# Kernel tuning notes

Measured on AMD Instinct MI355X. Metric: run time of the kernel, lower is better.

Reference implementation:

```python
import jax, jax.numpy as jnp
import numpy as np

T, C, H, W = 16, 3, 512, 512
PS, PT = 7, 1
NQ = 262144


def setup_inputs() -> dict:
    key = jax.random.key(0)
    k1, k2, k3, k4 = jax.random.split(key, 4)
    vid2fill = jnp.zeros((T, C, H, W), jnp.float32)
    patches = jax.random.normal(k1, (NQ, PT, C, PS, PS), jnp.float32)
    # queryInds columns: (t, h, w) top-left corners, each kept in-bounds
    qt = jax.random.randint(k2, (NQ, 1), 0, T - PT + 1)
    qh = jax.random.randint(k3, (NQ, 1), 0, H - PS + 1)
    qw = jax.random.randint(k4, (NQ, 1), 0, W - PS + 1)
    queryInds = jnp.concatenate([qt, qh, qw], axis=1).astype(jnp.int32)
    return {"vid2fill": vid2fill, "patches": patches, "queryInds": queryInds}


def reference(vid2fill, patches, queryInds):
    # vid2fill: [T,C,H,W]; patches: [N,pt,C,ps,ps]; queryInds: [N,3] = (t,h,w)
    T_, C_, H_, W_ = vid2fill.shape
    N, pt, _, ps, _ = patches.shape
    ti = queryInds[:, 0, None] + jnp.arange(pt)  # [N,pt]
    hi = queryInds[:, 1, None] + jnp.arange(ps)  # [N,ps]
    wi = queryInds[:, 2, None] + jnp.arange(ps)  # [N,ps]
    # flat spatial-temporal index over (t,h,w): [N,pt,ps,ps]
    flat = (ti[:, :, None, None] * H_ + hi[:, None, :, None]) * W_ + wi[:, None, None, :]
    # channels-last flat video [T*H*W, C] for a single vectorized scatter-add
    vid_flat = vid2fill.transpose(0, 2, 3, 1).reshape(-1, C_)
    p = patches.transpose(0, 1, 3, 4, 2).reshape(-1, C_)  # [N*pt*ps*ps, C]
    out = vid_flat.at[flat.reshape(-1)].add(p)
    return out.reshape(T_, H_, W_, C_).transpose(0, 3, 1, 2)
```

## Files before the change

### kernel.cpp

```cpp
#include <hip/hip_runtime.h>

constexpr int T_ = 16, C_ = 3, H_ = 512, W_ = 512, PS_ = 7;
constexpr int PATCH_ELEMS = C_ * PS_ * PS_;
constexpr int TILE  = 32;
constexpr int HALO  = PS_ - 1;
constexpr int LTILE = TILE + HALO;
constexpr int LSTRIDE = 40;
constexpr int NTH = H_ / TILE, NTW = W_ / TILE;
constexpr int NBINS = T_ * NTH * NTW;
constexpr int LDS_PER_C  = LTILE * LSTRIDE;
constexpr int ACC_FLOATS = C_ * LDS_PER_C;
constexpr int CAP = 160;
constexpr int BTHR = 192;
constexpr int CSTR = 16;
constexpr int NEX = 26 * 26;
constexpr int NSH = 192 + 156 + 420;

constexpr size_t OFF_COUNTS = 0;
constexpr size_t OFF_LIST   = (size_t)NBINS * CSTR * 4;
constexpr size_t WS_NEEDED  = OFF_LIST + (size_t)NBINS * CAP * 4;

__global__ void zero_counts_kernel(int* counts) {
    counts[blockIdx.x * 1024 + threadIdx.x] = 0;
}

__global__ void scatter_kernel(const int* __restrict__ q, int* __restrict__ counts,
                               int* __restrict__ list, int nq) {
    int n = blockIdx.x * 256 + threadIdx.x;
    if (n >= nq) return;
    int t = q[3 * n], h = q[3 * n + 1], w = q[3 * n + 2];
    int bin = (t * NTH + (h >> 5)) * NTW + (w >> 5);
    int pos = atomicAdd(counts + bin * CSTR, 1);
    if (pos < CAP) list[bin * CAP + pos] = (n << 10) | ((h & 31) << 5) | (w & 31);
}

__global__ __launch_bounds__(BTHR, 6) void accum_kernel(
    const float* __restrict__ patches, const int* __restrict__ counts,
    const int* __restrict__ list, float* __restrict__ out) {
    __shared__ float acc[ACC_FLOATS];
    __shared__ int recs[CAP];
    const int bin = blockIdx.x;
    const int t = bin >> 8;
    const int h0 = ((bin >> 4) & 15) * TILE, w0 = (bin & 15) * TILE;
    const int tid = threadIdx.x;
    const int lane = tid & 63, wid = tid >> 6;

    for (int i = tid; i < ACC_FLOATS; i += BTHR) acc[i] = 0.f;
    int cnt = counts[bin * CSTR];
    if (cnt > CAP) cnt = CAP;
    if (tid < cnt) recs[tid] = list[bin * CAP + tid];
    __syncthreads();

    {
        const int c = wid;
        const bool act = lane < PS_ * PS_;
        const int loff = act ? (lane / PS_) * LSTRIDE + (lane % PS_) : 0;
        float* __restrict__ ac = acc + c * LDS_PER_C;
        const float* __restrict__ pc = patches + c * (PS_ * PS_);

        float v0=0,v1=0,v2=0,v3=0,v4=0,v5=0,v6=0,v7=0;
        int o0=0,o1=0,o2=0,o3=0,o4=0,o5=0,o6=0,o7=0;
#define LDR(vv,oo,ii) { int rr = recs[(ii)]; \
        oo = ((rr >> 5) & 31) * LSTRIDE + (rr & 31) + loff; \
        vv = act ? pc[(size_t)(unsigned)(rr >> 10) * PATCH_ELEMS + lane] : 0.f; }
        if (0 < cnt) LDR(v0,o0, 0)
        if (1 < cnt) LDR(v1,o1, 1)
        if (2 < cnt) LDR(v2,o2, 2)
        if (3 < cnt) LDR(v3,o3, 3)
        if (4 < cnt) LDR(v4,o4, 4)
        if (5 < cnt) LDR(v5,o5, 5)
        if (6 < cnt) LDR(v6,o6, 6)
        if (7 < cnt) LDR(v7,o7, 7)
        for (int p = 0; p < cnt; p += 8) {
            float x0=v0,x1=v1,x2=v2,x3=v3,x4=v4,x5=v5,x6=v6,x7=v7;
            int q0=o0,q1=o1,q2=o2,q3=o3,q4=o4,q5=o5,q6=o6,q7=o7;
            int qq = p + 8;
            if (qq     < cnt) LDR(v0,o0, qq)
            if (qq + 1 < cnt) LDR(v1,o1, qq+1)
            if (qq + 2 < cnt) LDR(v2,o2, qq+2)
            if (qq + 3 < cnt) LDR(v3,o3, qq+3)
            if (qq + 4 < cnt) LDR(v4,o4, qq+4)
            if (qq + 5 < cnt) LDR(v5,o5, qq+5)
            if (qq + 6 < cnt) LDR(v6,o6, qq+6)
            if (qq + 7 < cnt) LDR(v7,o7, qq+7)
            if (act) {
                ac[q0] += x0;
                if (p + 1 < cnt) ac[q1] += x1;
                if (p + 2 < cnt) ac[q2] += x2;
                if (p + 3 < cnt) ac[q3] += x3;
                if (p + 4 < cnt) ac[q4] += x4;
                if (p + 5 < cnt) ac[q5] += x5;
                if (p + 6 < cnt) ac[q6] += x6;
                if (p + 7 < cnt) ac[q7] += x7;
            }
        }
#undef LDR
    }
    __syncthreads();

    const size_t obase = (size_t)t * C_ * H_ * W_;
    for (int k = tid; k < C_ * NEX; k += BTHR) {
        int c = k / NEX, r = k % NEX;
        int y = 6 + r / 26, x = 6 + r % 26;
        size_t g = obase + (size_t)c * (H_ * W_) + (size_t)(h0 + y) * W_ + (w0 + x);
        out[g] += acc[c * LDS_PER_C + y * LSTRIDE + x];
    }
    for (int k = tid; k < C_ * NSH; k += BTHR) {
        int c = k / NSH, r = k % NSH;
        int y, x;
        if (r < 192)      { y = r >> 5; x = r & 31; }
        else if (r < 348) { int r2 = r - 192; y = 6 + r2 / 6; x = r2 % 6; }
        else {
            int r2 = r - 348;
            if (r2 < 228) { y = TILE + r2 / LTILE; x = r2 % LTILE; }
            else          { int r3 = r2 - 228; y = r3 / HALO; x = TILE + r3 % HALO; }
        }
        float v = acc[c * LDS_PER_C + y * LSTRIDE + x];
        if (v != 0.f) {
            size_t g = obase + (size_t)c * (H_ * W_) + (size_t)(h0 + y) * W_ + (w0 + x);
            atomicAdd(out + g, v);
        }
    }
}

__global__ void scatter_add_kernel(const float* __restrict__ patches,
                                   const int* __restrict__ qinds,
                                   float* __restrict__ out, int total) {
    int tid = blockIdx.x * blockDim.x + threadIdx.x;
    if (tid >= total) return;
    int n = tid / PATCH_ELEMS;
    int r = tid - n * PATCH_ELEMS;
    int c = r / (PS_ * PS_);
    int rr = r - c * (PS_ * PS_);
    int ih = rr / PS_, iw = rr - ih * PS_;
    int t = qinds[n * 3 + 0], h = qinds[n * 3 + 1], w = qinds[n * 3 + 2];
    int out_idx = ((t * C_ + c) * H_ + (h + ih)) * W_ + (w + iw);
    atomicAdd(out + out_idx, patches[tid]);
}

extern "C" void kernel_launch(void* const* d_in, const int* in_sizes, int n_in,
                              void* d_out, int out_size, void* d_ws, size_t ws_size,
                              hipStream_t stream) {
    const float* vid     = (const float*)d_in[0];
    const float* patches = (const float*)d_in[1];
    const int*   qinds   = (const int*)d_in[2];
    float*       out     = (float*)d_out;
    const int nq = in_sizes[2] / 3;

    hipMemcpyAsync(out, vid, (size_t)out_size * sizeof(float),
                   hipMemcpyDeviceToDevice, stream);

    if (ws_size < WS_NEEDED) {
        int total = nq * PATCH_ELEMS;
        scatter_add_kernel<<<(total + 255) / 256, 256, 0, stream>>>(patches, qinds, out, total);
        return;
    }

    char* ws = (char*)d_ws;
    int* counts = (int*)(ws + OFF_COUNTS);
    int* list   = (int*)(ws + OFF_LIST);

    zero_counts_kernel<<<NBINS * CSTR / 1024, 1024, 0, stream>>>(counts);
    scatter_kernel<<<(nq + 255) / 256, 256, 0, stream>>>(qinds, counts, list, nq);
    accum_kernel<<<NBINS, BTHR, 0, stream>>>(patches, counts, list, out);
}
```

Baseline: 342.3 us.

## Gather patches from neighbor bins so each tile owns its output, drop atomics and memcpy

Each output tile block now collects records from its own bin and the three up/left neighbor bins whose patches can overlap it. It accumulates only its own 32x32 region in LDS and writes out = vid + acc with float4 stores. This removes the halo atomicAdds, the read-modify-write of out, and the separate device-to-device memcpy. The bin counters are no longer padded. In exchange, each patch is loaded by up to four blocks, there is an LDS atomic compaction pass, and patch loads are spent on elements that get masked off.

Result: faster. 306.1 us (-10.6%).

```diff
diff --git a/kernel.cpp b/kernel.cpp
--- a/kernel.cpp
+++ b/kernel.cpp
@@ -4,20 +4,18 @@
 constexpr int PATCH_ELEMS = C_ * PS_ * PS_;
 constexpr int TILE  = 32;
 constexpr int HALO  = PS_ - 1;
-constexpr int LTILE = TILE + HALO;
-constexpr int LSTRIDE = 40;
 constexpr int NTH = H_ / TILE, NTW = W_ / TILE;
 constexpr int NBINS = T_ * NTH * NTW;
-constexpr int LDS_PER_C  = LTILE * LSTRIDE;
-constexpr int ACC_FLOATS = C_ * LDS_PER_C;
+constexpr int ASTR = 36;
+constexpr int ACC_PER_C  = TILE * ASTR;
+constexpr int ACC_FLOATS = C_ * ACC_PER_C;
+constexpr int INTERIOR   = C_ * TILE * TILE;
 constexpr int CAP = 160;
+constexpr int RMAX = 4 * CAP;
 constexpr int BTHR = 192;
-constexpr int CSTR = 16;
-constexpr int NEX = 26 * 26;
-constexpr int NSH = 192 + 156 + 420;
 
 constexpr size_t OFF_COUNTS = 0;
-constexpr size_t OFF_LIST   = (size_t)NBINS * CSTR * 4;
+constexpr size_t OFF_LIST   = 16384;
 constexpr size_t WS_NEEDED  = OFF_LIST + (size_t)NBINS * CAP * 4;
 
 __global__ void zero_counts_kernel(int* counts) {
@@ -30,96 +28,111 @@
     if (n >= nq) return;
     int t = q[3 * n], h = q[3 * n + 1], w = q[3 * n + 2];
     int bin = (t * NTH + (h >> 5)) * NTW + (w >> 5);
-    int pos = atomicAdd(counts + bin * CSTR, 1);
+    int pos = atomicAdd(counts + bin, 1);
     if (pos < CAP) list[bin * CAP + pos] = (n << 10) | ((h & 31) << 5) | (w & 31);
 }
 
 __global__ __launch_bounds__(BTHR, 6) void accum_kernel(
     const float* __restrict__ patches, const int* __restrict__ counts,
-    const int* __restrict__ list, float* __restrict__ out) {
-    __shared__ float acc[ACC_FLOATS];
-    __shared__ int recs[CAP];
+    const int* __restrict__ list, const float* __restrict__ vid,
+    float* __restrict__ out) {
+    __shared__ alignas(16) float acc[ACC_FLOATS];
+    __shared__ int recs[RMAX];
+    __shared__ int nrec_sh;
     const int bin = blockIdx.x;
     const int t = bin >> 8;
-    const int h0 = ((bin >> 4) & 15) * TILE, w0 = (bin & 15) * TILE;
+    const int ti = (bin >> 4) & 15, tj = bin & 15;
+    const int h0 = ti * TILE, w0 = tj * TILE;
     const int tid = threadIdx.x;
     const int lane = tid & 63, wid = tid >> 6;
 
     for (int i = tid; i < ACC_FLOATS; i += BTHR) acc[i] = 0.f;
-    int cnt = counts[bin * CSTR];
-    if (cnt > CAP) cnt = CAP;
-    if (tid < cnt) recs[tid] = list[bin * CAP + tid];
+    if (tid == 0) nrec_sh = 0;
     __syncthreads();
+
+    {
+        const int srcs[4][2] = {{0, 0}, {-1, 0}, {0, -1}, {-1, -1}};
+#pragma unroll
+        for (int s = 0; s < 4; ++s) {
+            int di = srcs[s][0], dj = srcs[s][1];
+            if ((ti + di) < 0 || (tj + dj) < 0) continue;
+            int sbin = bin + di * NTW + dj;
+            int cs = counts[sbin];
+            if (cs > CAP) cs = CAP;
+            for (int k = tid; k < cs; k += BTHR) {
+                int rr = list[sbin * CAP + k];
+                int ry = ((rr >> 5) & 31) + di * TILE;
+                int rx = (rr & 31) + dj * TILE;
+                if (ry >= -HALO && rx >= -HALO) {
+                    int pos = atomicAdd(&nrec_sh, 1);
+                    if (pos < RMAX)
+                        recs[pos] = ((rr >> 10) << 12) | ((ry + 6) << 6) | (rx + 6);
+                }
+            }
+        }
+    }
+    __syncthreads();
+    int nrec = nrec_sh;
+    if (nrec > RMAX) nrec = RMAX;
 
     {
         const int c = wid;
         const bool act = lane < PS_ * PS_;
-        const int loff = act ? (lane / PS_) * LSTRIDE + (lane % PS_) : 0;
-        float* __restrict__ ac = acc + c * LDS_PER_C;
+        const int dy = lane / PS_, dx = lane % PS_;
+        float* __restrict__ ac = acc + c * ACC_PER_C;
         const float* __restrict__ pc = patches + c * (PS_ * PS_);
 
         float v0=0,v1=0,v2=0,v3=0,v4=0,v5=0,v6=0,v7=0;
-        int o0=0,o1=0,o2=0,o3=0,o4=0,o5=0,o6=0,o7=0;
+        int o0=-1,o1=-1,o2=-1,o3=-1,o4=-1,o5=-1,o6=-1,o7=-1;
 #define LDR(vv,oo,ii) { int rr = recs[(ii)]; \
-        oo = ((rr >> 5) & 31) * LSTRIDE + (rr & 31) + loff; \
-        vv = act ? pc[(size_t)(unsigned)(rr >> 10) * PATCH_ELEMS + lane] : 0.f; }
-        if (0 < cnt) LDR(v0,o0, 0)
-        if (1 < cnt) LDR(v1,o1, 1)
-        if (2 < cnt) LDR(v2,o2, 2)
-        if (3 < cnt) LDR(v3,o3, 3)
-        if (4 < cnt) LDR(v4,o4, 4)
-        if (5 < cnt) LDR(v5,o5, 5)
-        if (6 < cnt) LDR(v6,o6, 6)
-        if (7 < cnt) LDR(v7,o7, 7)
-        for (int p = 0; p < cnt; p += 8) {
+        int ty = ((rr >> 6) & 63) - 6 + dy; \
+        int tx = (rr & 63) - 6 + dx; \
+        bool ok = act && ((unsigned)ty < (unsigned)TILE) && ((unsigned)tx < (unsigned)TILE); \
+        oo = ok ? ty * ASTR + tx : -1; \
+        vv = act ? pc[(size_t)((unsigned)rr >> 12) * PATCH_ELEMS + lane] : 0.f; }
+        if (0 < nrec) LDR(v0,o0, 0)
+        if (1 < nrec) LDR(v1,o1, 1)
+        if (2 < nrec) LDR(v2,o2, 2)
+        if (3 < nrec) LDR(v3,o3, 3)
+        if (4 < nrec) LDR(v4,o4, 4)
+        if (5 < nrec) LDR(v5,o5, 5)
+        if (6 < nrec) LDR(v6,o6, 6)
+        if (7 < nrec) LDR(v7,o7, 7)
+        for (int p = 0; p < nrec; p += 8) {
             float x0=v0,x1=v1,x2=v2,x3=v3,x4=v4,x5=v5,x6=v6,x7=v7;
             int q0=o0,q1=o1,q2=o2,q3=o3,q4=o4,q5=o5,q6=o6,q7=o7;
             int qq = p + 8;
-            if (qq     < cnt) LDR(v0,o0, qq)
-            if (qq + 1 < cnt) LDR(v1,o1, qq+1)
-            if (qq + 2 < cnt) LDR(v2,o2, qq+2)
-            if (qq + 3 < cnt) LDR(v3,o3, qq+3)
-            if (qq + 4 < cnt) LDR(v4,o4, qq+4)
-            if (qq + 5 < cnt) LDR(v5,o5, qq+5)
-            if (qq + 6 < cnt) LDR(v6,o6, qq+6)
-            if (qq + 7 < cnt) LDR(v7,o7, qq+7)
-            if (act) {
-                ac[q0] += x0;
-                if (p + 1 < cnt) ac[q1] += x1;
-                if (p + 2 < cnt) ac[q2] += x2;
-                if (p + 3 < cnt) ac[q3] += x3;
-                if (p + 4 < cnt) ac[q4] += x4;
-                if (p + 5 < cnt) ac[q5] += x5;
-                if (p + 6 < cnt) ac[q6] += x6;
-                if (p + 7 < cnt) ac[q7] += x7;
-            }
+            o0=-1;o1=-1;o2=-1;o3=-1;o4=-1;o5=-1;o6=-1;o7=-1;
+            if (qq     < nrec) LDR(v0,o0, qq)
+            if (qq + 1 < nrec) LDR(v1,o1, qq+1)
+            if (qq + 2 < nrec) LDR(v2,o2, qq+2)
+            if (qq + 3 < nrec) LDR(v3,o3, qq+3)
+            if (qq + 4 < nrec) LDR(v4,o4, qq+4)
+            if (qq + 5 < nrec) LDR(v5,o5, qq+5)
+            if (qq + 6 < nrec) LDR(v6,o6, qq+6)
+            if (qq + 7 < nrec) LDR(v7,o7, qq+7)
+            if (q0 >= 0) ac[q0] += x0;
+            if (q1 >= 0 && p + 1 < nrec) ac[q1] += x1;
+            if (q2 >= 0 && p + 2 < nrec) ac[q2] += x2;
+            if (q3 >= 0 && p + 3 < nrec) ac[q3] += x3;
+            if (q4 >= 0 && p + 4 < nrec) ac[q4] += x4;
+            if (q5 >= 0 && p + 5 < nrec) ac[q5] += x5;
+            if (q6 >= 0 && p + 6 < nrec) ac[q6] += x6;
+            if (q7 >= 0 && p + 7 < nrec) ac[q7] += x7;
         }
 #undef LDR
     }
     __syncthreads();
 
     const size_t obase = (size_t)t * C_ * H_ * W_;
-    for (int k = tid; k < C_ * NEX; k += BTHR) {
-        int c = k / NEX, r = k % NEX;
-        int y = 6 + r / 26, x = 6 + r % 26;
-        size_t g = obase + (size_t)c * (H_ * W_) + (size_t)(h0 + y) * W_ + (w0 + x);
-        out[g] += acc[c * LDS_PER_C + y * LSTRIDE + x];
-    }
-    for (int k = tid; k < C_ * NSH; k += BTHR) {
-        int c = k / NSH, r = k % NSH;
-        int y, x;
-        if (r < 192)      { y = r >> 5; x = r & 31; }
-        else if (r < 348) { int r2 = r - 192; y = 6 + r2 / 6; x = r2 % 6; }
-        else {
-            int r2 = r - 348;
-            if (r2 < 228) { y = TILE + r2 / LTILE; x = r2 % LTILE; }
-            else          { int r3 = r2 - 228; y = r3 / HALO; x = TILE + r3 % HALO; }
-        }
-        float v = acc[c * LDS_PER_C + y * LSTRIDE + x];
-        if (v != 0.f) {
-            size_t g = obase + (size_t)c * (H_ * W_) + (size_t)(h0 + y) * W_ + (w0 + x);
-            atomicAdd(out + g, v);
-        }
+    for (int i = tid; i < INTERIOR / 4; i += BTHR) {
+        int cc = i >> 8, rem = i & 255, y = rem >> 3, x4 = rem & 7;
+        size_t g = obase + (size_t)cc * (H_ * W_) + (size_t)(h0 + y) * W_ + (w0 + x4 * 4);
+        const float4 vv = *reinterpret_cast<const float4*>(vid + g);
+        const float4 aa = *reinterpret_cast<const float4*>(
+            &acc[cc * ACC_PER_C + y * ASTR + x4 * 4]);
+        float4 r; r.x = vv.x + aa.x; r.y = vv.y + aa.y; r.z = vv.z + aa.z; r.w = vv.w + aa.w;
+        *reinterpret_cast<float4*>(out + g) = r;
     }
 }
 
@@ -147,10 +160,9 @@
     float*       out     = (float*)d_out;
     const int nq = in_sizes[2] / 3;
 
-    hipMemcpyAsync(out, vid, (size_t)out_size * sizeof(float),
-                   hipMemcpyDeviceToDevice, stream);
-
     if (ws_size < WS_NEEDED) {
+        hipMemcpyAsync(out, vid, (size_t)out_size * sizeof(float),
+                       hipMemcpyDeviceToDevice, stream);
         int total = nq * PATCH_ELEMS;
         scatter_add_kernel<<<(total + 255) / 256, 256, 0, stream>>>(patches, qinds, out, total);
         return;
@@ -160,7 +172,7 @@
     int* counts = (int*)(ws + OFF_COUNTS);
     int* list   = (int*)(ws + OFF_LIST);
 
-    zero_counts_kernel<<<NBINS * CSTR / 1024, 1024, 0, stream>>>(counts);
+    zero_counts_kernel<<<NBINS / 1024, 1024, 0, stream>>>(counts);
     scatter_kernel<<<(nq + 255) / 256, 256, 0, stream>>>(qinds, counts, list, nq);
-    accum_kernel<<<NBINS, BTHR, 0, stream>>>(patches, counts, list, out);
+    accum_kernel<<<NBINS, BTHR, 0, stream>>>(patches, counts, list, vid, out);
 }
```
